# Kernel tuning notes

Hardware: AMD Instinct MI355X
Metric: run time of the kernel (lower is better)

## Reference

```python
import jax, jax.numpy as jnp
import numpy as np

B, IN, H, OUT = 32768, 64, 256, 768
HM, TS = 4, 64  # hm_modalities, timestep_size; OUT = 3*HM*TS


def setup_inputs() -> dict:
    key = jax.random.key(0)
    ks = jax.random.split(key, 24)
    def w(k, shape):
        scale = 1.0 / np.sqrt(shape[0])
        return jax.random.normal(k, shape, jnp.float32) * scale
    inp = jax.random.normal(ks[0], (B, IN), jnp.float32)
    state1 = jax.random.normal(ks[1], (B, 2 * H), jnp.float32)
    state2 = jax.random.normal(ks[2], (B, 2 * H), jnp.float32)
    d = {"inp": inp, "state1": state1, "state2": state2}
    names = ["wf", "wk", "wi", "ws"]
    for i, n in enumerate(names):
        d[f"l1_{n}"] = w(ks[3 + i], (IN + H, H))
        d[f"l1_b{n[1]}"] = jnp.zeros((H,), jnp.float32)
        d[f"l2_{n}"] = w(ks[7 + i], (H + H, H))
        d[f"l2_b{n[1]}"] = jnp.zeros((H,), jnp.float32)
    d["ff_w"] = w(ks[11], (H, OUT))
    return d


def lstm_cell(state, x_in, wf, bf, wk, bk, wi, bi, ws, bs):
    h = wf.shape[1]
    prev_out = state[:, :h]
    cell = state[:, h:]
    x = jnp.concatenate([x_in, prev_out], axis=1)
    reset = jax.nn.sigmoid(x @ wf + bf)
    write = jax.nn.sigmoid(x @ wk + bk)
    interm = jnp.tanh(x @ wi + bi)
    read = jax.nn.sigmoid(x @ ws + bs)
    cell = reset * cell + write * interm
    out = read * jnp.tanh(cell)
    return out, jnp.concatenate([out, cell], axis=1)


def reference(inp, state1, state2,
              l1_wf, l1_bf, l1_wk, l1_bk, l1_wi, l1_bi, l1_ws, l1_bs,
              l2_wf, l2_bf, l2_wk, l2_bk, l2_wi, l2_bi, l2_ws, l2_bs,
              ff_w):
    out, new_state1 = lstm_cell(state1, inp, l1_wf, l1_bf, l1_wk, l1_bk,
                                l1_wi, l1_bi, l1_ws, l1_bs)
    out, new_state2 = lstm_cell(state2, out, l2_wf, l2_bf, l2_wk, l2_bk,
                                l2_wi, l2_bi, l2_ws, l2_bs)
    out = out @ ff_w  # [B, OUT]
    third = OUT // 3
    means = out[:, :third]
    deviances = jnp.exp(out[:, third:2 * third])
    mult = out[:, -third:].reshape(B, HM, TS)
    mult = jax.nn.softmax(mult, axis=1).reshape(B, HM * TS)
    return means, deviances, mult, new_state1, new_state2
```

## Files before the change

### kernel.cpp

```cpp
#include <hip/hip_runtime.h>


typedef __attribute__((ext_vector_type(8))) short short8;
typedef __attribute__((ext_vector_type(4))) short short4_t;
typedef __attribute__((ext_vector_type(4))) float floatx4;

#define BATCH 32768

static const size_t DEV_OFF  = (size_t)BATCH * 256;
static const size_t MULT_OFF = (size_t)2 * BATCH * 256;
static const size_t NS1_OFF  = (size_t)3 * BATCH * 256;
static const size_t NS2_OFF  = NS1_OFF + (size_t)BATCH * 512;

static const size_t W1P = 0;
static const size_t W2P = (size_t)1024 * 320;
static const size_t W3P = W2P + (size_t)1024 * 512;
static const size_t X1O = W3P + (size_t)768 * 256;
static const size_t X2O = X1O + (size_t)BATCH * 320;
static const size_t X3O = X2O + (size_t)BATCH * 512;

__device__ __forceinline__ unsigned short f2bf(float f) {
    union { float f; unsigned int i; } v; v.f = f;
    unsigned int i = v.i;
    i += 0x7fff + ((i >> 16) & 1);
    return (unsigned short)(i >> 16);
}
__device__ __forceinline__ float sigmoidf_(float x) {
    return 1.f / (1.f + __expf(-x));
}
__device__ __forceinline__ float tanhf_(float x) {
    float e = __expf(2.f * x);
    return 1.f - 2.f / (e + 1.f);
}

__device__ __forceinline__ void gl_lds16(const unsigned short* g,
                                         unsigned short* l) {
    __builtin_amdgcn_global_load_lds(
        (const __attribute__((address_space(1))) unsigned int*)g,
        (__attribute__((address_space(3))) unsigned int*)l,
        16, 0, 0);
}

__global__ __launch_bounds__(256) void pack_all(
    const float* __restrict__ inp, const float* __restrict__ s1,
    const float* __restrict__ s2,
    const float* __restrict__ w10, const float* __restrict__ w11,
    const float* __restrict__ w12, const float* __restrict__ w13,
    const float* __restrict__ w20, const float* __restrict__ w21,
    const float* __restrict__ w22, const float* __restrict__ w23,
    const float* __restrict__ fw, unsigned short* __restrict__ ws)
{
    const int q = blockIdx.x * 256 + threadIdx.x;
    if (q < 524288) {
        int r = q >> 4, c = (q & 15) << 2;
        float4 v = *(const float4*)(inp + (size_t)r * 64 + c);
        short4_t h;
        h.x = (short)f2bf(v.x); h.y = (short)f2bf(v.y);
        h.z = (short)f2bf(v.z); h.w = (short)f2bf(v.w);
        *(short4_t*)(ws + X1O + (size_t)r * 320 + c) = h;
    } else if (q < 2621440) {
        int j = q - 524288;
        int r = j >> 6, c = (j & 63) << 2;
        float4 v = *(const float4*)(s1 + (size_t)r * 512 + c);
        short4_t h;
        h.x = (short)f2bf(v.x); h.y = (short)f2bf(v.y);
        h.z = (short)f2bf(v.z); h.w = (short)f2bf(v.w);
        *(short4_t*)(ws + X1O + (size_t)r * 320 + 64 + c) = h;
    } else if (q < 4718592) {
        int j = q - 2621440;
        int r = j >> 6, c = (j & 63) << 2;
        float4 v = *(const float4*)(s2 + (size_t)r * 512 + c);
        short4_t h;
        h.x = (short)f2bf(v.x); h.y = (short)f2bf(v.y);
        h.z = (short)f2bf(v.z); h.w = (short)f2bf(v.w);
        *(short4_t*)(ws + X2O + (size_t)r * 512 + 256 + c) = h;
    } else if (q < 4800512) {
        int j = q - 4718592;
        int n = j / 80, k = (j % 80) << 2;
        int h = n >> 2, g = n & 3;
        const float* s = g == 0 ? w10 : g == 1 ? w11 : g == 2 ? w12 : w13;
        short4_t o;
        o.x = (short)f2bf(s[(size_t)(k + 0) * 256 + h]);
        o.y = (short)f2bf(s[(size_t)(k + 1) * 256 + h]);
        o.z = (short)f2bf(s[(size_t)(k + 2) * 256 + h]);
        o.w = (short)f2bf(s[(size_t)(k + 3) * 256 + h]);
        *(short4_t*)(ws + W1P + (size_t)n * 320 + k) = o;
    } else if (q < 4931584) {
        int j = q - 4800512;
        int n = j >> 7, k = (j & 127) << 2;
        int h = n >> 2, g = n & 3;
        const float* s = g == 0 ? w20 : g == 1 ? w21 : g == 2 ? w22 : w23;
        short4_t o;
        o.x = (short)f2bf(s[(size_t)(k + 0) * 256 + h]);
        o.y = (short)f2bf(s[(size_t)(k + 1) * 256 + h]);
        o.z = (short)f2bf(s[(size_t)(k + 2) * 256 + h]);
        o.w = (short)f2bf(s[(size_t)(k + 3) * 256 + h]);
        *(short4_t*)(ws + W2P + (size_t)n * 512 + k) = o;
    } else {
        int j = q - 4931584;
        int n = j >> 6, k = (j & 63) << 2;
        int col = (n < 512) ? n : (512 + ((n & 3) << 6) + ((n - 512) >> 2));
        short4_t o;
        o.x = (short)f2bf(fw[(size_t)(k + 0) * 768 + col]);
        o.y = (short)f2bf(fw[(size_t)(k + 1) * 768 + col]);
        o.z = (short)f2bf(fw[(size_t)(k + 2) * 768 + col]);
        o.w = (short)f2bf(fw[(size_t)(k + 3) * 768 + col]);
        *(short4_t*)(ws + W3P + (size_t)n * 256 + k) = o;
    }
}

template<int KT, int XST>
__global__ __launch_bounds__(256) void lstm_gemm(
    const unsigned short* __restrict__ xin,
    const unsigned short* __restrict__ wp,
    const float* __restrict__ b0, const float* __restrict__ b1,
    const float* __restrict__ b2, const float* __restrict__ b3,
    const float* __restrict__ state,
    float* __restrict__ nstate,
    unsigned short* __restrict__ xnext)
{
    __shared__ __align__(16) union {
        struct { unsigned short a[128][64]; unsigned short b[128][64]; } st;
        float ep[128][68];
    } lds;
    __shared__ float sbias[4][32];

    const int tid  = threadIdx.x;
    const int w    = tid >> 6;
    const int lane = tid & 63;
    const int lhi  = lane >> 4, llo = lane & 15;
    const int wr   = w >> 1, wc = w & 1;
    const int nt   = blockIdx.x;
    const int row0 = blockIdx.y * 128;
    const int nc0  = nt * 128;
    const int hbase = nt * 32;

    if (tid < 128) {
        int g = tid >> 5, hl = tid & 31;
        const float* bp = g == 0 ? b0 : g == 1 ? b1 : g == 2 ? b2 : b3;
        sbias[g][hl] = bp[hbase + hl];
    }

    floatx4 acc[4][4];
#pragma unroll
    for (int i = 0; i < 4; i++)
#pragma unroll
        for (int j = 0; j < 4; j++) acc[i][j] = (floatx4){0.f, 0.f, 0.f, 0.f};

    const int arow  = (w << 5) + (lane >> 3);
    const int acolb = (lane & 7) << 3;
    const unsigned short* agp = xin + (size_t)(row0 + arow) * KT + acolb;
    const unsigned short* bgp = wp  + (size_t)(nc0 + arow) * KT + acolb;

    for (int c = 0; c < KT / 64; ++c) {
        const int kb = c << 6;
#pragma unroll
        for (int p = 0; p < 4; ++p) {
            gl_lds16(agp + (size_t)(p * 8) * KT + kb,
                     &lds.st.a[(w << 5) + (p << 3)][0]);
            gl_lds16(bgp + (size_t)(p * 8) * KT + kb,
                     &lds.st.b[(w << 5) + (p << 3)][0]);
        }
        __syncthreads();
#pragma unroll
        for (int ks = 0; ks < 2; ++ks) {
            const int k8 = ks * 32 + lhi * 8;
            short8 a[4], b[4];
#pragma unroll
            for (int mi = 0; mi < 4; mi++)
                a[mi] = *(const short8*)&lds.st.a[wr * 64 + mi * 16 + llo][k8];
#pragma unroll
            for (int ni = 0; ni < 4; ni++)
                b[ni] = *(const short8*)&lds.st.b[wc * 64 + ni * 16 + llo][k8];
#pragma unroll
            for (int mi = 0; mi < 4; mi++)
#pragma unroll
                for (int ni = 0; ni < 4; ni++)
                    acc[mi][ni] = __builtin_amdgcn_mfma_f32_16x16x32_bf16(
                        a[mi], b[ni], acc[mi][ni], 0, 0, 0);
        }
        __syncthreads();
    }

    for (int pass = 0; pass < 2; ++pass) {
        if (pass) __syncthreads();
        if (wc == pass) {
#pragma unroll
            for (int mi = 0; mi < 4; mi++)
#pragma unroll
                for (int ni = 0; ni < 4; ni++)
#pragma unroll
                    for (int r = 0; r < 4; r++)
                        lds.ep[wr * 64 + mi * 16 + lhi * 4 + r]
                              [ni * 16 + llo] = acc[mi][ni][r];
        }
        __syncthreads();
        const int hl   = tid & 15;
        const int hblk = pass * 16 + hl;
        const int hg   = hbase + hblk;
        const float bf_ = sbias[0][hblk], bk_ = sbias[1][hblk];
        const float bi_ = sbias[2][hblk], bs_ = sbias[3][hblk];
#pragma unroll
        for (int rr = 0; rr < 8; ++rr) {
            const int r = (tid >> 4) + rr * 16;
            float4 z = *(const float4*)&lds.ep[r][hl << 2];
            float rst = sigmoidf_(z.x + bf_);
            float wrt = sigmoidf_(z.y + bk_);
            float itm = tanhf_(z.z + bi_);
            float rd  = sigmoidf_(z.w + bs_);
            const size_t rowel = (size_t)(row0 + r) * 512;
            float cold = state[rowel + 256 + hg];
            float cell = rst * cold + wrt * itm;
            float o = rd * tanhf_(cell);
            nstate[rowel + hg]       = o;
            nstate[rowel + 256 + hg] = cell;
            xnext[(size_t)(row0 + r) * XST + hg] = f2bf(o);
        }
    }
}

__global__ __launch_bounds__(256) void ff_gemm(
    const unsigned short* __restrict__ xin,
    const unsigned short* __restrict__ wp,
    float* __restrict__ out)
{
    __shared__ __align__(16) union {
        struct { unsigned short a[128][64]; unsigned short b[128][64]; } st;
        float ep[128][68];
    } lds;

    const int tid  = threadIdx.x;
    const int w    = tid >> 6;
    const int lane = tid & 63;
    const int lhi  = lane >> 4, llo = lane & 15;
    const int wr   = w >> 1, wc = w & 1;
    const int nt   = blockIdx.x;
    const int row0 = blockIdx.y * 128;
    const int nc0  = nt * 128;

    floatx4 acc[4][4];
#pragma unroll
    for (int i = 0; i < 4; i++)
#pragma unroll
        for (int j = 0; j < 4; j++) acc[i][j] = (floatx4){0.f, 0.f, 0.f, 0.f};

    const int arow  = (w << 5) + (lane >> 3);
    const int acolb = (lane & 7) << 3;
    const unsigned short* agp = xin + (size_t)(row0 + arow) * 256 + acolb;
    const unsigned short* bgp = wp  + (size_t)(nc0 + arow) * 256 + acolb;

    for (int c = 0; c < 4; ++c) {
        const int kb = c << 6;
#pragma unroll
        for (int p = 0; p < 4; ++p) {
            gl_lds16(agp + (size_t)(p * 8) * 256 + kb,
                     &lds.st.a[(w << 5) + (p << 3)][0]);
            gl_lds16(bgp + (size_t)(p * 8) * 256 + kb,
                     &lds.st.b[(w << 5) + (p << 3)][0]);
        }
        __syncthreads();
#pragma unroll
        for (int ks = 0; ks < 2; ++ks) {
            const int k8 = ks * 32 + lhi * 8;
            short8 a[4], b[4];
#pragma unroll
            for (int mi = 0; mi < 4; mi++)
                a[mi] = *(const short8*)&lds.st.a[wr * 64 + mi * 16 + llo][k8];
#pragma unroll
            for (int ni = 0; ni < 4; ni++)
                b[ni] = *(const short8*)&lds.st.b[wc * 64 + ni * 16 + llo][k8];
#pragma unroll
            for (int mi = 0; mi < 4; mi++)
#pragma unroll
                for (int ni = 0; ni < 4; ni++)
                    acc[mi][ni] = __builtin_amdgcn_mfma_f32_16x16x32_bf16(
                        a[mi], b[ni], acc[mi][ni], 0, 0, 0);
        }
        __syncthreads();
    }

    if (nt < 4) {
        const bool dev = (nt >= 2);
        float* obase = out + (dev ? DEV_OFF : (size_t)0);
        const int cb = (nt & 1) * 128 + wc * 64;
#pragma unroll
        for (int mi = 0; mi < 4; mi++)
#pragma unroll
            for (int ni = 0; ni < 4; ni++) {
                const int cc = cb + ni * 16 + llo;
#pragma unroll
                for (int r = 0; r < 4; r++) {
                    const int m = wr * 64 + mi * 16 + lhi * 4 + r;
                    float v = acc[mi][ni][r];
                    if (dev) v = __expf(v);
                    obase[(size_t)(row0 + m) * 256 + cc] = v;
                }
            }
    } else {
        const int tb = (nt - 4) * 32;
        for (int pass = 0; pass < 2; ++pass) {
            if (pass) __syncthreads();
            if (wc == pass) {
#pragma unroll
                for (int mi = 0; mi < 4; mi++)
#pragma unroll
                    for (int ni = 0; ni < 4; ni++)
#pragma unroll
                        for (int r = 0; r < 4; r++)
                            lds.ep[wr * 64 + mi * 16 + lhi * 4 + r]
                                  [ni * 16 + llo] = acc[mi][ni][r];
            }
            __syncthreads();
            const int tl = tid & 15;
#pragma unroll
            for (int rr = 0; rr < 8; ++rr) {
                const int r = (tid >> 4) + rr * 16;
                float4 z = *(const float4*)&lds.ep[r][tl << 2];
                float mx = fmaxf(fmaxf(z.x, z.y), fmaxf(z.z, z.w));
                float e0 = __expf(z.x - mx), e1 = __expf(z.y - mx);
                float e2 = __expf(z.z - mx), e3 = __expf(z.w - mx);
                float inv = 1.f / (e0 + e1 + e2 + e3);
                size_t base = MULT_OFF + (size_t)(row0 + r) * 256
                            + tb + pass * 16 + tl;
                out[base]       = e0 * inv;
                out[base + 64]  = e1 * inv;
                out[base + 128] = e2 * inv;
                out[base + 192] = e3 * inv;
            }
        }
    }
}

extern "C" void kernel_launch(void* const* d_in, const int* in_sizes, int n_in,
                              void* d_out, int out_size, void* d_ws, size_t ws_size,
                              hipStream_t stream)
{
    typedef const float* cfp;
    cfp inp = (cfp)d_in[0];
    cfp st1 = (cfp)d_in[1];
    cfp st2 = (cfp)d_in[2];
    cfp l1w0 = (cfp)d_in[3],  l1w1 = (cfp)d_in[7],  l1w2 = (cfp)d_in[11], l1w3 = (cfp)d_in[15];
    cfp l1b0 = (cfp)d_in[4],  l1b1 = (cfp)d_in[8],  l1b2 = (cfp)d_in[12], l1b3 = (cfp)d_in[16];
    cfp l2w0 = (cfp)d_in[5],  l2w1 = (cfp)d_in[9],  l2w2 = (cfp)d_in[13], l2w3 = (cfp)d_in[17];
    cfp l2b0 = (cfp)d_in[6],  l2b1 = (cfp)d_in[10], l2b2 = (cfp)d_in[14], l2b3 = (cfp)d_in[18];
    cfp ffw = (cfp)d_in[19];

    float* out = (float*)d_out;
    unsigned short* ws = (unsigned short*)d_ws;

    pack_all<<<19456, 256, 0, stream>>>(inp, st1, st2,
                                        l1w0, l1w1, l1w2, l1w3,
                                        l2w0, l2w1, l2w2, l2w3, ffw, ws);

    lstm_gemm<320, 512><<<dim3(8, 256), 256, 0, stream>>>(
        ws + X1O, ws + W1P, l1b0, l1b1, l1b2, l1b3,
        st1, out + NS1_OFF, ws + X2O);

    lstm_gemm<512, 256><<<dim3(8, 256), 256, 0, stream>>>(
        ws + X2O, ws + W2P, l2b0, l2b1, l2b2, l2b3,
        st2, out + NS2_OFF, ws + X3O);

    ff_gemm<<<dim3(6, 256), 256, 0, stream>>>(ws + X3O, ws + W3P, out);
}
```

Before: 518.1 us.

## Interleave packed weight columns so gate epilogues run from registers, remap blocks per XCD

The packed weight layout is reordered so that each 16-column MFMA tile holds a single gate (or modality) for 16 hidden units. Each lane therefore owns all four gates of one hidden unit directly in its accumulators. This removes the LDS round-trip, the extra barriers and the bias staging from the LSTM and softmax epilogues. The launches also become 1D with an XCD-aware block-to-tile mapping, so that consecutive row tiles share an XCD's L2. In exchange, the epilogue global stores become less coalesced, with 16-wide column runs per row.

```diff
diff --git a/kernel.cpp b/kernel.cpp
--- a/kernel.cpp
+++ b/kernel.cpp
@@ -77,29 +77,37 @@
     } else if (q < 4800512) {
         int j = q - 4718592;
         int n = j / 80, k = (j % 80) << 2;
-        int h = n >> 2, g = n & 3;
+        int hh = ((n >> 6) << 4) + (n & 15);
+        int g = (n >> 4) & 3;
         const float* s = g == 0 ? w10 : g == 1 ? w11 : g == 2 ? w12 : w13;
         short4_t o;
-        o.x = (short)f2bf(s[(size_t)(k + 0) * 256 + h]);
-        o.y = (short)f2bf(s[(size_t)(k + 1) * 256 + h]);
-        o.z = (short)f2bf(s[(size_t)(k + 2) * 256 + h]);
-        o.w = (short)f2bf(s[(size_t)(k + 3) * 256 + h]);
+        o.x = (short)f2bf(s[(size_t)(k + 0) * 256 + hh]);
+        o.y = (short)f2bf(s[(size_t)(k + 1) * 256 + hh]);
+        o.z = (short)f2bf(s[(size_t)(k + 2) * 256 + hh]);
+        o.w = (short)f2bf(s[(size_t)(k + 3) * 256 + hh]);
         *(short4_t*)(ws + W1P + (size_t)n * 320 + k) = o;
     } else if (q < 4931584) {
         int j = q - 4800512;
         int n = j >> 7, k = (j & 127) << 2;
-        int h = n >> 2, g = n & 3;
+        int hh = ((n >> 6) << 4) + (n & 15);
+        int g = (n >> 4) & 3;
         const float* s = g == 0 ? w20 : g == 1 ? w21 : g == 2 ? w22 : w23;
         short4_t o;
-        o.x = (short)f2bf(s[(size_t)(k + 0) * 256 + h]);
-        o.y = (short)f2bf(s[(size_t)(k + 1) * 256 + h]);
-        o.z = (short)f2bf(s[(size_t)(k + 2) * 256 + h]);
-        o.w = (short)f2bf(s[(size_t)(k + 3) * 256 + h]);
+        o.x = (short)f2bf(s[(size_t)(k + 0) * 256 + hh]);
+        o.y = (short)f2bf(s[(size_t)(k + 1) * 256 + hh]);
+        o.z = (short)f2bf(s[(size_t)(k + 2) * 256 + hh]);
+        o.w = (short)f2bf(s[(size_t)(k + 3) * 256 + hh]);
         *(short4_t*)(ws + W2P + (size_t)n * 512 + k) = o;
     } else {
         int j = q - 4931584;
         int n = j >> 6, k = (j & 63) << 2;
-        int col = (n < 512) ? n : (512 + ((n & 3) << 6) + ((n - 512) >> 2));
+        int col;
+        if (n < 512) col = n;
+        else {
+            int t = (((n - 512) >> 6) << 4) + (n & 15);
+            int m = (n >> 4) & 3;
+            col = 512 + m * 64 + t;
+        }
         short4_t o;
         o.x = (short)f2bf(fw[(size_t)(k + 0) * 768 + col]);
         o.y = (short)f2bf(fw[(size_t)(k + 1) * 768 + col]);
@@ -119,27 +127,23 @@
     float* __restrict__ nstate,
     unsigned short* __restrict__ xnext)
 {
-    __shared__ __align__(16) union {
-        struct { unsigned short a[128][64]; unsigned short b[128][64]; } st;
-        float ep[128][68];
+    __shared__ __align__(16) struct {
+        unsigned short a[128][64];
+        unsigned short b[128][64];
     } lds;
-    __shared__ float sbias[4][32];
 
     const int tid  = threadIdx.x;
     const int w    = tid >> 6;
     const int lane = tid & 63;
     const int lhi  = lane >> 4, llo = lane & 15;
     const int wr   = w >> 1, wc = w & 1;
-    const int nt   = blockIdx.x;
-    const int row0 = blockIdx.y * 128;
+
+    const int lin  = blockIdx.x;
+    const int xcd  = lin & 7;
+    const int kk   = lin >> 3;
+    const int nt   = kk & 7;
+    const int row0 = (xcd * 32 + (kk >> 3)) * 128;
     const int nc0  = nt * 128;
-    const int hbase = nt * 32;
-
-    if (tid < 128) {
-        int g = tid >> 5, hl = tid & 31;
-        const float* bp = g == 0 ? b0 : g == 1 ? b1 : g == 2 ? b2 : b3;
-        sbias[g][hl] = bp[hbase + hl];
-    }
 
     floatx4 acc[4][4];
 #pragma unroll
@@ -157,9 +161,9 @@
 #pragma unroll
         for (int p = 0; p < 4; ++p) {
             gl_lds16(agp + (size_t)(p * 8) * KT + kb,
-                     &lds.st.a[(w << 5) + (p << 3)][0]);
+                     &lds.a[(w << 5) + (p << 3)][0]);
             gl_lds16(bgp + (size_t)(p * 8) * KT + kb,
-                     &lds.st.b[(w << 5) + (p << 3)][0]);
+                     &lds.b[(w << 5) + (p << 3)][0]);
         }
         __syncthreads();
 #pragma unroll
@@ -168,10 +172,10 @@
             short8 a[4], b[4];
 #pragma unroll
             for (int mi = 0; mi < 4; mi++)
-                a[mi] = *(const short8*)&lds.st.a[wr * 64 + mi * 16 + llo][k8];
+                a[mi] = *(const short8*)&lds.a[wr * 64 + mi * 16 + llo][k8];
 #pragma unroll
             for (int ni = 0; ni < 4; ni++)
-                b[ni] = *(const short8*)&lds.st.b[wc * 64 + ni * 16 + llo][k8];
+                b[ni] = *(const short8*)&lds.b[wc * 64 + ni * 16 + llo][k8];
 #pragma unroll
             for (int mi = 0; mi < 4; mi++)
 #pragma unroll
@@ -182,41 +186,25 @@
         __syncthreads();
     }
 
-    for (int pass = 0; pass < 2; ++pass) {
-        if (pass) __syncthreads();
-        if (wc == pass) {
-#pragma unroll
-            for (int mi = 0; mi < 4; mi++)
-#pragma unroll
-                for (int ni = 0; ni < 4; ni++)
-#pragma unroll
-                    for (int r = 0; r < 4; r++)
-                        lds.ep[wr * 64 + mi * 16 + lhi * 4 + r]
-                              [ni * 16 + llo] = acc[mi][ni][r];
-        }
-        __syncthreads();
-        const int hl   = tid & 15;
-        const int hblk = pass * 16 + hl;
-        const int hg   = hbase + hblk;
-        const float bf_ = sbias[0][hblk], bk_ = sbias[1][hblk];
-        const float bi_ = sbias[2][hblk], bs_ = sbias[3][hblk];
-#pragma unroll
-        for (int rr = 0; rr < 8; ++rr) {
-            const int r = (tid >> 4) + rr * 16;
-            float4 z = *(const float4*)&lds.ep[r][hl << 2];
-            float rst = sigmoidf_(z.x + bf_);
-            float wrt = sigmoidf_(z.y + bk_);
-            float itm = tanhf_(z.z + bi_);
-            float rd  = sigmoidf_(z.w + bs_);
-            const size_t rowel = (size_t)(row0 + r) * 512;
-            float cold = state[rowel + 256 + hg];
+    const int h = nt * 32 + wc * 16 + llo;
+    const float bf_ = b0[h], bk_ = b1[h], bi_ = b2[h], bs_ = b3[h];
+#pragma unroll
+    for (int mi = 0; mi < 4; mi++)
+#pragma unroll
+        for (int r = 0; r < 4; r++) {
+            const int m = wr * 64 + mi * 16 + lhi * 4 + r;
+            const size_t rowel = (size_t)(row0 + m) * 512;
+            float rst = sigmoidf_(acc[mi][0][r] + bf_);
+            float wrt = sigmoidf_(acc[mi][1][r] + bk_);
+            float itm = tanhf_(acc[mi][2][r] + bi_);
+            float rd  = sigmoidf_(acc[mi][3][r] + bs_);
+            float cold = state[rowel + 256 + h];
             float cell = rst * cold + wrt * itm;
             float o = rd * tanhf_(cell);
-            nstate[rowel + hg]       = o;
-            nstate[rowel + 256 + hg] = cell;
-            xnext[(size_t)(row0 + r) * XST + hg] = f2bf(o);
-        }
-    }
+            nstate[rowel + h]       = o;
+            nstate[rowel + 256 + h] = cell;
+            xnext[(size_t)(row0 + m) * XST + h] = f2bf(o);
+        }
 }
 
 __global__ __launch_bounds__(256) void ff_gemm(
@@ -224,9 +212,9 @@
     const unsigned short* __restrict__ wp,
     float* __restrict__ out)
 {
-    __shared__ __align__(16) union {
-        struct { unsigned short a[128][64]; unsigned short b[128][64]; } st;
-        float ep[128][68];
+    __shared__ __align__(16) struct {
+        unsigned short a[128][64];
+        unsigned short b[128][64];
     } lds;
 
     const int tid  = threadIdx.x;
@@ -234,8 +222,12 @@
     const int lane = tid & 63;
     const int lhi  = lane >> 4, llo = lane & 15;
     const int wr   = w >> 1, wc = w & 1;
-    const int nt   = blockIdx.x;
-    const int row0 = blockIdx.y * 128;
+
+    const int lin  = blockIdx.x;
+    const int xcd  = lin & 7;
+    const int kk   = lin >> 3;
+    const int nt   = kk % 6;
+    const int row0 = (xcd * 32 + kk / 6) * 128;
     const int nc0  = nt * 128;
 
     floatx4 acc[4][4];
@@ -254,9 +246,9 @@
 #pragma unroll
         for (int p = 0; p < 4; ++p) {
             gl_lds16(agp + (size_t)(p * 8) * 256 + kb,
-                     &lds.st.a[(w << 5) + (p << 3)][0]);
+                     &lds.a[(w << 5) + (p << 3)][0]);
             gl_lds16(bgp + (size_t)(p * 8) * 256 + kb,
-                     &lds.st.b[(w << 5) + (p << 3)][0]);
+                     &lds.b[(w << 5) + (p << 3)][0]);
         }
         __syncthreads();
 #pragma unroll
@@ -265,10 +257,10 @@
             short8 a[4], b[4];
 #pragma unroll
             for (int mi = 0; mi < 4; mi++)
-                a[mi] = *(const short8*)&lds.st.a[wr * 64 + mi * 16 + llo][k8];
+                a[mi] = *(const short8*)&lds.a[wr * 64 + mi * 16 + llo][k8];
 #pragma unroll
             for (int ni = 0; ni < 4; ni++)
-                b[ni] = *(const short8*)&lds.st.b[wc * 64 + ni * 16 + llo][k8];
+                b[ni] = *(const short8*)&lds.b[wc * 64 + ni * 16 + llo][k8];
 #pragma unroll
             for (int mi = 0; mi < 4; mi++)
 #pragma unroll
@@ -297,37 +289,24 @@
                 }
             }
     } else {
-        const int tb = (nt - 4) * 32;
-        for (int pass = 0; pass < 2; ++pass) {
-            if (pass) __syncthreads();
-            if (wc == pass) {
-#pragma unroll
-                for (int mi = 0; mi < 4; mi++)
-#pragma unroll
-                    for (int ni = 0; ni < 4; ni++)
-#pragma unroll
-                        for (int r = 0; r < 4; r++)
-                            lds.ep[wr * 64 + mi * 16 + lhi * 4 + r]
-                                  [ni * 16 + llo] = acc[mi][ni][r];
-            }
-            __syncthreads();
-            const int tl = tid & 15;
-#pragma unroll
-            for (int rr = 0; rr < 8; ++rr) {
-                const int r = (tid >> 4) + rr * 16;
-                float4 z = *(const float4*)&lds.ep[r][tl << 2];
-                float mx = fmaxf(fmaxf(z.x, z.y), fmaxf(z.z, z.w));
-                float e0 = __expf(z.x - mx), e1 = __expf(z.y - mx);
-                float e2 = __expf(z.z - mx), e3 = __expf(z.w - mx);
+        const int t = (nt - 4) * 32 + wc * 16 + llo;
+#pragma unroll
+        for (int mi = 0; mi < 4; mi++)
+#pragma unroll
+            for (int r = 0; r < 4; r++) {
+                const int mrow = wr * 64 + mi * 16 + lhi * 4 + r;
+                float v0 = acc[mi][0][r], v1 = acc[mi][1][r];
+                float v2 = acc[mi][2][r], v3 = acc[mi][3][r];
+                float mx = fmaxf(fmaxf(v0, v1), fmaxf(v2, v3));
+                float e0 = __expf(v0 - mx), e1 = __expf(v1 - mx);
+                float e2 = __expf(v2 - mx), e3 = __expf(v3 - mx);
                 float inv = 1.f / (e0 + e1 + e2 + e3);
-                size_t base = MULT_OFF + (size_t)(row0 + r) * 256
-                            + tb + pass * 16 + tl;
+                size_t base = MULT_OFF + (size_t)(row0 + mrow) * 256 + t;
                 out[base]       = e0 * inv;
                 out[base + 64]  = e1 * inv;
                 out[base + 128] = e2 * inv;
                 out[base + 192] = e3 * inv;
             }
-        }
     }
 }
 
@@ -352,13 +331,13 @@
                                         l1w0, l1w1, l1w2, l1w3,
                                         l2w0, l2w1, l2w2, l2w3, ffw, ws);
 
-    lstm_gemm<320, 512><<<dim3(8, 256), 256, 0, stream>>>(
+    lstm_gemm<320, 512><<<2048, 256, 0, stream>>>(
         ws + X1O, ws + W1P, l1b0, l1b1, l1b2, l1b3,
         st1, out + NS1_OFF, ws + X2O);
 
-    lstm_gemm<512, 256><<<dim3(8, 256), 256, 0, stream>>>(
+    lstm_gemm<512, 256><<<2048, 256, 0, stream>>>(
         ws + X2O, ws + W2P, l2b0, l2b1, l2b2, l2b3,
         st2, out + NS2_OFF, ws + X3O);
 
-    ff_gemm<<<dim3(6, 256), 256, 0, stream>>>(ws + X3O, ws + W3P, out);
-}
+    ff_gemm<<<1536, 256, 0, stream>>>(ws + X3O, ws + W3P, out);
+}
```

New measurement: 506.3 us. 2.3% less time.
